# Optimization experiments

Measured on AMD Instinct MI355X. Metric: run time of the kernel, lower is better.

Reference implementation:

```python
import jax, jax.numpy as jnp
import numpy as np

N_NODES, E, M_CELLS = 100000, 400000, 50000
D_IN, D_H, D_OUT = 384, 256, 256


def setup_inputs() -> dict:
    key = jax.random.key(0)
    ks = jax.random.split(key, 13)
    s = 0.02
    return {
        "chunk_features": jax.random.normal(ks[0], (N_NODES, D_IN), jnp.float32),
        "flat_nodes_t": jax.random.randint(ks[1], (E,), 0, N_NODES),
        "cell_asgn_t": jax.random.randint(ks[2], (E,), 0, M_CELLS),
        "M": M_CELLS,
        # phi: Linear(D_IN,D_H)+ReLU, Linear(D_H,D_H)+ReLU
        "W1": jax.random.normal(ks[3], (D_IN, D_H), jnp.float32) * s,
        "b1": jnp.zeros((D_H,), jnp.float32),
        "W2": jax.random.normal(ks[4], (D_H, D_H), jnp.float32) * s,
        "b2": jnp.zeros((D_H,), jnp.float32),
        # rho: Linear(D_H,D_H)+ReLU, Linear(D_H,D_H)+ReLU, Linear(D_H,D_OUT)
        "R1": jax.random.normal(ks[5], (D_H, D_H), jnp.float32) * s,
        "c1": jnp.zeros((D_H,), jnp.float32),
        "R2": jax.random.normal(ks[6], (D_H, D_H), jnp.float32) * s,
        "c2": jnp.zeros((D_H,), jnp.float32),
        "R3": jax.random.normal(ks[7], (D_H, D_OUT), jnp.float32) * s,
        "c3": jnp.zeros((D_OUT,), jnp.float32),
    }


def reference(chunk_features, flat_nodes_t, cell_asgn_t, M,
              W1, b1, W2, b2, R1, c1, R2, c2, R3, c3):
    # gather node features per cell-membership: [E, D_IN]
    x = chunk_features[flat_nodes_t]
    # phi MLP
    h = jax.nn.relu(x @ W1 + b1)
    h = jax.nn.relu(h @ W2 + b2)            # [E, D_H]
    # scatter-add per cell (torch scatter_add_ into zeros)
    cell_sums = jax.ops.segment_sum(h, cell_asgn_t, num_segments=M)  # [M, D_H]
    # rho MLP
    r = jax.nn.relu(cell_sums @ R1 + c1)
    r = jax.nn.relu(r @ R2 + c2)
    return r @ R3 + c3                      # [M, D_OUT]
```

## Files before the change

kernel.cpp:

```cpp
#include <hip/hip_runtime.h>

typedef unsigned short u16;
typedef __bf16 bf16x8 __attribute__((ext_vector_type(8)));
typedef float f32x4 __attribute__((ext_vector_type(4)));

__device__ __forceinline__ u16 f2bf(float f) {
  unsigned int u = __builtin_bit_cast(unsigned int, f);
  u += 0x7fffu + ((u >> 16) & 1u);
  return (u16)(u >> 16);
}
__device__ __forceinline__ float bf2f(u16 h) {
  unsigned int u = ((unsigned int)h) << 16;
  return __builtin_bit_cast(float, u);
}

__global__ __launch_bounds__(256) void k_prep(
    const float* __restrict__ W1, const float* __restrict__ W2,
    const float* __restrict__ R1, const float* __restrict__ R2, const float* __restrict__ R3,
    u16* __restrict__ W1s, u16* __restrict__ W2s,
    u16* __restrict__ R1s, u16* __restrict__ R2s, u16* __restrict__ R3s) {
  int t = blockIdx.x * 256 + threadIdx.x;
  const float* src; u16* dst; int lt;
  if (t < 12288) { src = W1; dst = W1s; lt = t; }
  else {
    int u = t - 12288;
    int m = u >> 13;
    lt = u & 8191;
    if (m == 0)      { src = W2; dst = W2s; }
    else if (m == 1) { src = R1; dst = R1s; }
    else if (m == 2) { src = R2; dst = R2s; }
    else if (m == 3) { src = R3; dst = R3s; }
    else return;
  }
  int lane = lt & 63;
  int nt = (lt >> 6) & 15;
  int ks = lt >> 10;
  int col = nt * 16 + (lane & 15);
  int kb = ks * 32 + (lane >> 4) * 8;
  union { u16 u[8]; uint4 v; } o;
#pragma unroll
  for (int j = 0; j < 8; ++j) o.u[j] = f2bf(src[(size_t)(kb + j) * 256 + col]);
  *(uint4*)(dst + (size_t)lt * 8) = o.v;
}

__global__ __launch_bounds__(256) void k_hist(const int* __restrict__ cells,
                                              int* __restrict__ counts, int E) {
  int e = blockIdx.x * 256 + threadIdx.x;
  if (e < E) atomicAdd(&counts[cells[e]], 1);
}

__global__ __launch_bounds__(256) void k_scan1(const int* __restrict__ counts,
                                               int* __restrict__ offs,
                                               int* __restrict__ bsum, int M) {
  __shared__ int ws[4];
  int tid = threadIdx.x, lane = tid & 63, wid = tid >> 6;
  int i = blockIdx.x * 256 + tid;
  int v = (i < M) ? counts[i] : 0;
  int x = v;
#pragma unroll
  for (int s = 1; s < 64; s <<= 1) { int y = __shfl_up(x, s); if (lane >= s) x += y; }
  if (lane == 63) ws[wid] = x;
  __syncthreads();
  int pre = 0;
#pragma unroll
  for (int w = 0; w < 4; ++w) if (w < wid) pre += ws[w];
  if (i < M) offs[i] = pre + x - v;
  if (tid == 255) bsum[blockIdx.x] = pre + x;
}

__global__ __launch_bounds__(256) void k_scan2(int* __restrict__ bsum, int nb) {
  __shared__ int ws[4];
  int tid = threadIdx.x, lane = tid & 63, wid = tid >> 6;
  int v = (tid < nb) ? bsum[tid] : 0;
  int x = v;
#pragma unroll
  for (int s = 1; s < 64; s <<= 1) { int y = __shfl_up(x, s); if (lane >= s) x += y; }
  if (lane == 63) ws[wid] = x;
  __syncthreads();
  int pre = 0;
#pragma unroll
  for (int w = 0; w < 4; ++w) if (w < wid) pre += ws[w];
  if (tid < nb) bsum[tid] = pre + x - v;
}

__global__ __launch_bounds__(256) void k_scan3(int* __restrict__ offs,
                                               const int* __restrict__ bsum,
                                               int* __restrict__ cursor, int M, int E) {
  int i = blockIdx.x * 256 + threadIdx.x;
  if (i < M) { int o = offs[i] + bsum[blockIdx.x]; offs[i] = o; cursor[i] = o; }
  if (i == M) offs[M] = E;
}

__global__ __launch_bounds__(256) void k_scatter(const int* __restrict__ cells,
                                                 const int* __restrict__ nodes,
                                                 int* __restrict__ cursor,
                                                 int* __restrict__ sorted, int E) {
  int e = blockIdx.x * 256 + threadIdx.x;
  if (e < E) {
    int c = cells[e];
    int p = atomicAdd(&cursor[c], 1);
    sorted[p] = nodes[e];
  }
}

__global__ __launch_bounds__(256, 2) void k_phi(
    const float* __restrict__ X,
    const u16* __restrict__ W1s, const float* __restrict__ b1,
    const u16* __restrict__ W2s, const float* __restrict__ b2,
    u16* __restrict__ H, int N) {
  __shared__ __align__(16) u16 stage[64 * 256];
  __shared__ __align__(16) u16 hbuf[64 * 256];
  const int tid = threadIdx.x, lane = tid & 63, wid = tid >> 6;
  const int g = lane >> 4, r16 = lane & 15;
  const int rbase = blockIdx.x * 64;

  f32x4 acc[4][4];
#pragma unroll
  for (int m = 0; m < 4; ++m)
#pragma unroll
    for (int n = 0; n < 4; ++n) acc[m][n] = (f32x4){0.f, 0.f, 0.f, 0.f};

#pragma unroll
  for (int ph = 0; ph < 2; ++ph) {
    if (ph) __syncthreads();
    if (ph == 0) {
#pragma unroll
      for (int it = 0; it < 16; ++it) {
        int u = it * 256 + tid;
        int row = u >> 6, c4 = u & 63;
        int crow = rbase + row; crow = crow < N ? crow : N - 1;
        f32x4 v = *(const f32x4*)(X + (size_t)crow * 384 + c4 * 4);
        uint2 pk;
        pk.x = (unsigned int)f2bf(v[0]) | ((unsigned int)f2bf(v[1]) << 16);
        pk.y = (unsigned int)f2bf(v[2]) | ((unsigned int)f2bf(v[3]) << 16);
        *(uint2*)(stage + row * 256 + ((c4 * 4) ^ ((row & 15) << 3))) = pk;
      }
    } else {
#pragma unroll
      for (int it = 0; it < 8; ++it) {
        int u = it * 256 + tid;
        int row = u >> 5, c4 = u & 31;
        int crow = rbase + row; crow = crow < N ? crow : N - 1;
        f32x4 v = *(const f32x4*)(X + (size_t)crow * 384 + 256 + c4 * 4);
        uint2 pk;
        pk.x = (unsigned int)f2bf(v[0]) | ((unsigned int)f2bf(v[1]) << 16);
        pk.y = (unsigned int)f2bf(v[2]) | ((unsigned int)f2bf(v[3]) << 16);
        *(uint2*)(stage + row * 256 + ((c4 * 4) ^ ((row & 15) << 3))) = pk;
      }
    }
    __syncthreads();
    const int nks = ph ? 4 : 8;
    const int ksg0 = ph ? 8 : 0;
#pragma unroll
    for (int ksl = 0; ksl < nks; ++ksl) {
      int ks = ksg0 + ksl;
      bf16x8 bfr[4];
#pragma unroll
      for (int n = 0; n < 4; ++n)
        bfr[n] = *(const bf16x8*)(W1s + ((size_t)(ks * 16 + wid * 4 + n) * 64 + lane) * 8);
#pragma unroll
      for (int m = 0; m < 4; ++m) {
        int row = m * 16 + r16;
        bf16x8 af = *(const bf16x8*)(stage + row * 256 + ((ksl * 32 + g * 8) ^ (r16 << 3)));
#pragma unroll
        for (int n = 0; n < 4; ++n)
          acc[m][n] = __builtin_amdgcn_mfma_f32_16x16x32_bf16(af, bfr[n], acc[m][n], 0, 0, 0);
      }
    }
  }

  float bias1[4];
#pragma unroll
  for (int n = 0; n < 4; ++n) bias1[n] = b1[wid * 64 + n * 16 + r16];
#pragma unroll
  for (int m = 0; m < 4; ++m)
#pragma unroll
    for (int n = 0; n < 4; ++n)
#pragma unroll
      for (int rr = 0; rr < 4; ++rr) {
        int row = m * 16 + g * 4 + rr;
        int col = wid * 64 + n * 16 + r16;
        float v = fmaxf(acc[m][n][rr] + bias1[n], 0.f);
        hbuf[row * 256 + (col ^ ((row & 15) << 3))] = f2bf(v);
      }
  __syncthreads();

  f32x4 acc2[4][4];
#pragma unroll
  for (int m = 0; m < 4; ++m)
#pragma unroll
    for (int n = 0; n < 4; ++n) acc2[m][n] = (f32x4){0.f, 0.f, 0.f, 0.f};
#pragma unroll
  for (int ks = 0; ks < 8; ++ks) {
    bf16x8 bfr[4];
#pragma unroll
    for (int n = 0; n < 4; ++n)
      bfr[n] = *(const bf16x8*)(W2s + ((size_t)(ks * 16 + wid * 4 + n) * 64 + lane) * 8);
#pragma unroll
    for (int m = 0; m < 4; ++m) {
      int row = m * 16 + r16;
      bf16x8 af = *(const bf16x8*)(hbuf + row * 256 + ((ks * 32 + g * 8) ^ (r16 << 3)));
#pragma unroll
      for (int n = 0; n < 4; ++n)
        acc2[m][n] = __builtin_amdgcn_mfma_f32_16x16x32_bf16(af, bfr[n], acc2[m][n], 0, 0, 0);
    }
  }

  float bias2[4];
#pragma unroll
  for (int n = 0; n < 4; ++n) bias2[n] = b2[wid * 64 + n * 16 + r16];
#pragma unroll
  for (int m = 0; m < 4; ++m)
#pragma unroll
    for (int n = 0; n < 4; ++n)
#pragma unroll
      for (int rr = 0; rr < 4; ++rr) {
        int row = m * 16 + g * 4 + rr;
        int col = wid * 64 + n * 16 + r16;
        float v = fmaxf(acc2[m][n][rr] + bias2[n], 0.f);
        stage[row * 256 + (col ^ ((row & 15) << 3))] = f2bf(v);
      }
  __syncthreads();

#pragma unroll
  for (int it = 0; it < 8; ++it) {
    int u = it * 256 + tid;
    int row = u >> 5, k8 = u & 31;
    uint4 d = *(const uint4*)(stage + row * 256 + ((k8 * 8) ^ ((row & 15) << 3)));
    int grow = rbase + row;
    if (grow < N) *(uint4*)(H + (size_t)grow * 256 + k8 * 8) = d;
  }
}

__global__ __launch_bounds__(256) void k_cellsum(
    const u16* __restrict__ H, const int* __restrict__ sorted,
    const int* __restrict__ offs, u16* __restrict__ CS, int M) {
  const int lane = threadIdx.x & 63, wid = threadIdx.x >> 6;
  int c = blockIdx.x * 4 + wid;
  if (c >= M) return;
  int s = offs[c], e = offs[c + 1];
  float a0 = 0.f, a1 = 0.f, a2 = 0.f, a3 = 0.f;
  for (int i = s; i < e; ++i) {
    int node = sorted[i];
    ushort4 h = *(const ushort4*)(H + (size_t)node * 256 + lane * 4);
    a0 += bf2f(h.x); a1 += bf2f(h.y); a2 += bf2f(h.z); a3 += bf2f(h.w);
  }
  ushort4 o;
  o.x = f2bf(a0); o.y = f2bf(a1); o.z = f2bf(a2); o.w = f2bf(a3);
  *(ushort4*)(CS + (size_t)c * 256 + lane * 4) = o;
}

__global__ __launch_bounds__(256, 2) void k_rho(
    const u16* __restrict__ CS,
    const u16* __restrict__ R1s, const float* __restrict__ c1,
    const u16* __restrict__ R2s, const float* __restrict__ c2,
    const u16* __restrict__ R3s, const float* __restrict__ c3,
    float* __restrict__ OUT, int M) {
  __shared__ __align__(16) u16 stage[64 * 256];
  __shared__ __align__(16) u16 hbuf[64 * 256];
  const int tid = threadIdx.x, lane = tid & 63, wid = tid >> 6;
  const int g = lane >> 4, r16 = lane & 15;
  const int rbase = blockIdx.x * 64;

#pragma unroll
  for (int it = 0; it < 8; ++it) {
    int u = it * 256 + tid;
    int row = u >> 5, k8 = u & 31;
    int crow = rbase + row; crow = crow < M ? crow : M - 1;
    uint4 d = *(const uint4*)(CS + (size_t)crow * 256 + k8 * 8);
    *(uint4*)(stage + row * 256 + ((k8 * 8) ^ ((row & 15) << 3))) = d;
  }
  __syncthreads();

  f32x4 acc[4][4];
#pragma unroll
  for (int m = 0; m < 4; ++m)
#pragma unroll
    for (int n = 0; n < 4; ++n) acc[m][n] = (f32x4){0.f, 0.f, 0.f, 0.f};
#pragma unroll
  for (int ks = 0; ks < 8; ++ks) {
    bf16x8 bfr[4];
#pragma unroll
    for (int n = 0; n < 4; ++n)
      bfr[n] = *(const bf16x8*)(R1s + ((size_t)(ks * 16 + wid * 4 + n) * 64 + lane) * 8);
#pragma unroll
    for (int m = 0; m < 4; ++m) {
      int row = m * 16 + r16;
      bf16x8 af = *(const bf16x8*)(stage + row * 256 + ((ks * 32 + g * 8) ^ (r16 << 3)));
#pragma unroll
      for (int n = 0; n < 4; ++n)
        acc[m][n] = __builtin_amdgcn_mfma_f32_16x16x32_bf16(af, bfr[n], acc[m][n], 0, 0, 0);
    }
  }
  float bias1[4];
#pragma unroll
  for (int n = 0; n < 4; ++n) bias1[n] = c1[wid * 64 + n * 16 + r16];
#pragma unroll
  for (int m = 0; m < 4; ++m)
#pragma unroll
    for (int n = 0; n < 4; ++n)
#pragma unroll
      for (int rr = 0; rr < 4; ++rr) {
        int row = m * 16 + g * 4 + rr;
        int col = wid * 64 + n * 16 + r16;
        float v = fmaxf(acc[m][n][rr] + bias1[n], 0.f);
        hbuf[row * 256 + (col ^ ((row & 15) << 3))] = f2bf(v);
      }
  __syncthreads();

  f32x4 acc2[4][4];
#pragma unroll
  for (int m = 0; m < 4; ++m)
#pragma unroll
    for (int n = 0; n < 4; ++n) acc2[m][n] = (f32x4){0.f, 0.f, 0.f, 0.f};
#pragma unroll
  for (int ks = 0; ks < 8; ++ks) {
    bf16x8 bfr[4];
#pragma unroll
    for (int n = 0; n < 4; ++n)
      bfr[n] = *(const bf16x8*)(R2s + ((size_t)(ks * 16 + wid * 4 + n) * 64 + lane) * 8);
#pragma unroll
    for (int m = 0; m < 4; ++m) {
      int row = m * 16 + r16;
      bf16x8 af = *(const bf16x8*)(hbuf + row * 256 + ((ks * 32 + g * 8) ^ (r16 << 3)));
#pragma unroll
      for (int n = 0; n < 4; ++n)
        acc2[m][n] = __builtin_amdgcn_mfma_f32_16x16x32_bf16(af, bfr[n], acc2[m][n], 0, 0, 0);
    }
  }
  float bias2[4];
#pragma unroll
  for (int n = 0; n < 4; ++n) bias2[n] = c2[wid * 64 + n * 16 + r16];
#pragma unroll
  for (int m = 0; m < 4; ++m)
#pragma unroll
    for (int n = 0; n < 4; ++n)
#pragma unroll
      for (int rr = 0; rr < 4; ++rr) {
        int row = m * 16 + g * 4 + rr;
        int col = wid * 64 + n * 16 + r16;
        float v = fmaxf(acc2[m][n][rr] + bias2[n], 0.f);
        stage[row * 256 + (col ^ ((row & 15) << 3))] = f2bf(v);
      }
  __syncthreads();

  f32x4 acc3[4][4];
#pragma unroll
  for (int m = 0; m < 4; ++m)
#pragma unroll
    for (int n = 0; n < 4; ++n) acc3[m][n] = (f32x4){0.f, 0.f, 0.f, 0.f};
#pragma unroll
  for (int ks = 0; ks < 8; ++ks) {
    bf16x8 bfr[4];
#pragma unroll
    for (int n = 0; n < 4; ++n)
      bfr[n] = *(const bf16x8*)(R3s + ((size_t)(ks * 16 + wid * 4 + n) * 64 + lane) * 8);
#pragma unroll
    for (int m = 0; m < 4; ++m) {
      int row = m * 16 + r16;
      bf16x8 af = *(const bf16x8*)(stage + row * 256 + ((ks * 32 + g * 8) ^ (r16 << 3)));
#pragma unroll
      for (int n = 0; n < 4; ++n)
        acc3[m][n] = __builtin_amdgcn_mfma_f32_16x16x32_bf16(af, bfr[n], acc3[m][n], 0, 0, 0);
    }
  }
#pragma unroll
  for (int n = 0; n < 4; ++n) {
    float bias = c3[wid * 64 + n * 16 + r16];
#pragma unroll
    for (int m = 0; m < 4; ++m)
#pragma unroll
      for (int rr = 0; rr < 4; ++rr) {
        int grow = rbase + m * 16 + g * 4 + rr;
        if (grow < M) OUT[(size_t)grow * 256 + wid * 64 + n * 16 + r16] = acc3[m][n][rr] + bias;
      }
  }
}

extern "C" void kernel_launch(void* const* d_in, const int* in_sizes, int n_in,
                              void* d_out, int out_size, void* d_ws, size_t ws_size,
                              hipStream_t stream) {
  const float* X    = (const float*)d_in[0];
  const int* nodes  = (const int*)d_in[1];
  const int* cells  = (const int*)d_in[2];
  const float* W1   = (const float*)d_in[4];
  const float* b1   = (const float*)d_in[5];
  const float* W2   = (const float*)d_in[6];
  const float* b2   = (const float*)d_in[7];
  const float* R1   = (const float*)d_in[8];
  const float* c1   = (const float*)d_in[9];
  const float* R2   = (const float*)d_in[10];
  const float* c2   = (const float*)d_in[11];
  const float* R3   = (const float*)d_in[12];
  const float* c3   = (const float*)d_in[13];
  float* OUT = (float*)d_out;

  const int N = in_sizes[0] / 384;
  const int E = in_sizes[1];
  const int M = out_size / 256;

  char* ws = (char*)d_ws;
  size_t off = 0;
  auto alloc = [&](size_t b) { size_t o = off; off += (b + 255) & ~(size_t)255; return o; };
  u16* W1s    = (u16*)(ws + alloc((size_t)12 * 16 * 64 * 8 * 2));
  u16* W2s    = (u16*)(ws + alloc((size_t)8 * 16 * 64 * 8 * 2));
  u16* R1s    = (u16*)(ws + alloc((size_t)8 * 16 * 64 * 8 * 2));
  u16* R2s    = (u16*)(ws + alloc((size_t)8 * 16 * 64 * 8 * 2));
  u16* R3s    = (u16*)(ws + alloc((size_t)8 * 16 * 64 * 8 * 2));
  u16* H      = (u16*)(ws + alloc((size_t)N * 256 * 2));
  u16* CS     = (u16*)(ws + alloc((size_t)M * 256 * 2));
  int* counts = (int*)(ws + alloc((size_t)M * 4));
  int* offs   = (int*)(ws + alloc((size_t)(M + 1) * 4));
  int* cursor = (int*)(ws + alloc((size_t)M * 4));
  int* sorted = (int*)(ws + alloc((size_t)E * 4));
  int* bsum   = (int*)(ws + alloc((size_t)256 * 4));

  const int NB = (M + 255) / 256;

  hipMemsetAsync(counts, 0, (size_t)M * 4, stream);
  k_prep<<<176, 256, 0, stream>>>(W1, W2, R1, R2, R3, W1s, W2s, R1s, R2s, R3s);
  k_hist<<<(E + 255) / 256, 256, 0, stream>>>(cells, counts, E);
  k_scan1<<<NB, 256, 0, stream>>>(counts, offs, bsum, M);
  k_scan2<<<1, 256, 0, stream>>>(bsum, NB);
  k_scan3<<<(M + 256) / 256, 256, 0, stream>>>(offs, bsum, cursor, M, E);
  k_scatter<<<(E + 255) / 256, 256, 0, stream>>>(cells, nodes, cursor, sorted, E);
  k_phi<<<(N + 63) / 64, 256, 0, stream>>>(X, W1s, b1, W2s, b2, H, N);
  k_cellsum<<<(M + 3) / 4, 256, 0, stream>>>(H, sorted, offs, CS, M);
  k_rho<<<(M + 63) / 64, 256, 0, stream>>>(CS, R1s, c1, R2s, c2, R3s, c3, OUT, M);
}
```

Before: 232.6 us.

## Single LDS buffer, weight-fragment prefetch, and batched index gather in cellsum

```diff
diff --git a/kernel.cpp b/kernel.cpp
--- a/kernel.cpp
+++ b/kernel.cpp
@@ -103,71 +103,98 @@
   }
 }
 
-__global__ __launch_bounds__(256, 2) void k_phi(
+__global__ __launch_bounds__(256, 4) void k_phi(
     const float* __restrict__ X,
     const u16* __restrict__ W1s, const float* __restrict__ b1,
     const u16* __restrict__ W2s, const float* __restrict__ b2,
     u16* __restrict__ H, int N) {
-  __shared__ __align__(16) u16 stage[64 * 256];
-  __shared__ __align__(16) u16 hbuf[64 * 256];
+  __shared__ __align__(16) u16 buf[64 * 256];
   const int tid = threadIdx.x, lane = tid & 63, wid = tid >> 6;
   const int g = lane >> 4, r16 = lane & 15;
   const int rbase = blockIdx.x * 64;
 
+  const u16* w1p = W1s + (size_t)(wid * 4) * 512 + lane * 8;
+  const u16* w2p = W2s + (size_t)(wid * 4) * 512 + lane * 8;
+
   f32x4 acc[4][4];
 #pragma unroll
   for (int m = 0; m < 4; ++m)
 #pragma unroll
     for (int n = 0; n < 4; ++n) acc[m][n] = (f32x4){0.f, 0.f, 0.f, 0.f};
 
-#pragma unroll
-  for (int ph = 0; ph < 2; ++ph) {
-    if (ph) __syncthreads();
-    if (ph == 0) {
-#pragma unroll
-      for (int it = 0; it < 16; ++it) {
-        int u = it * 256 + tid;
-        int row = u >> 6, c4 = u & 63;
-        int crow = rbase + row; crow = crow < N ? crow : N - 1;
-        f32x4 v = *(const f32x4*)(X + (size_t)crow * 384 + c4 * 4);
-        uint2 pk;
-        pk.x = (unsigned int)f2bf(v[0]) | ((unsigned int)f2bf(v[1]) << 16);
-        pk.y = (unsigned int)f2bf(v[2]) | ((unsigned int)f2bf(v[3]) << 16);
-        *(uint2*)(stage + row * 256 + ((c4 * 4) ^ ((row & 15) << 3))) = pk;
-      }
+  bf16x8 bfr[4];
+#pragma unroll
+  for (int n = 0; n < 4; ++n) bfr[n] = *(const bf16x8*)(w1p + n * 512);
+
+#pragma unroll
+  for (int it = 0; it < 16; ++it) {
+    int u = it * 256 + tid;
+    int row = u >> 6, c4 = u & 63;
+    int crow = rbase + row; crow = crow < N ? crow : N - 1;
+    f32x4 v = *(const f32x4*)(X + (size_t)crow * 384 + c4 * 4);
+    uint2 pk;
+    pk.x = (unsigned int)f2bf(v[0]) | ((unsigned int)f2bf(v[1]) << 16);
+    pk.y = (unsigned int)f2bf(v[2]) | ((unsigned int)f2bf(v[3]) << 16);
+    *(uint2*)(buf + row * 256 + ((c4 * 4) ^ ((row & 15) << 3))) = pk;
+  }
+  __syncthreads();
+
+#pragma unroll
+  for (int ksl = 0; ksl < 8; ++ksl) {
+    bf16x8 bnx[4];
+#pragma unroll
+    for (int n = 0; n < 4; ++n)
+      bnx[n] = *(const bf16x8*)(w1p + (size_t)(ksl + 1) * 8192 + n * 512);
+#pragma unroll
+    for (int m = 0; m < 4; ++m) {
+      int row = m * 16 + r16;
+      bf16x8 af = *(const bf16x8*)(buf + row * 256 + ((ksl * 32 + g * 8) ^ (r16 << 3)));
+#pragma unroll
+      for (int n = 0; n < 4; ++n)
+        acc[m][n] = __builtin_amdgcn_mfma_f32_16x16x32_bf16(af, bfr[n], acc[m][n], 0, 0, 0);
+    }
+#pragma unroll
+    for (int n = 0; n < 4; ++n) bfr[n] = bnx[n];
+  }
+  __syncthreads();
+
+#pragma unroll
+  for (int it = 0; it < 8; ++it) {
+    int u = it * 256 + tid;
+    int row = u >> 5, c4 = u & 31;
+    int crow = rbase + row; crow = crow < N ? crow : N - 1;
+    f32x4 v = *(const f32x4*)(X + (size_t)crow * 384 + 256 + c4 * 4);
+    uint2 pk;
+    pk.x = (unsigned int)f2bf(v[0]) | ((unsigned int)f2bf(v[1]) << 16);
+    pk.y = (unsigned int)f2bf(v[2]) | ((unsigned int)f2bf(v[3]) << 16);
+    *(uint2*)(buf + row * 256 + ((c4 * 4) ^ ((row & 15) << 3))) = pk;
+  }
+  __syncthreads();
+
+#pragma unroll
+  for (int ksl = 0; ksl < 4; ++ksl) {
+    bf16x8 bnx[4];
+    if (ksl < 3) {
+#pragma unroll
+      for (int n = 0; n < 4; ++n)
+        bnx[n] = *(const bf16x8*)(w1p + (size_t)(9 + ksl) * 8192 + n * 512);
     } else {
 #pragma unroll
-      for (int it = 0; it < 8; ++it) {
-        int u = it * 256 + tid;
-        int row = u >> 5, c4 = u & 31;
-        int crow = rbase + row; crow = crow < N ? crow : N - 1;
-        f32x4 v = *(const f32x4*)(X + (size_t)crow * 384 + 256 + c4 * 4);
-        uint2 pk;
-        pk.x = (unsigned int)f2bf(v[0]) | ((unsigned int)f2bf(v[1]) << 16);
-        pk.y = (unsigned int)f2bf(v[2]) | ((unsigned int)f2bf(v[3]) << 16);
-        *(uint2*)(stage + row * 256 + ((c4 * 4) ^ ((row & 15) << 3))) = pk;
-      }
-    }
-    __syncthreads();
-    const int nks = ph ? 4 : 8;
-    const int ksg0 = ph ? 8 : 0;
-#pragma unroll
-    for (int ksl = 0; ksl < nks; ++ksl) {
-      int ks = ksg0 + ksl;
-      bf16x8 bfr[4];
-#pragma unroll
-      for (int n = 0; n < 4; ++n)
-        bfr[n] = *(const bf16x8*)(W1s + ((size_t)(ks * 16 + wid * 4 + n) * 64 + lane) * 8);
-#pragma unroll
-      for (int m = 0; m < 4; ++m) {
-        int row = m * 16 + r16;
-        bf16x8 af = *(const bf16x8*)(stage + row * 256 + ((ksl * 32 + g * 8) ^ (r16 << 3)));
-#pragma unroll
-        for (int n = 0; n < 4; ++n)
-          acc[m][n] = __builtin_amdgcn_mfma_f32_16x16x32_bf16(af, bfr[n], acc[m][n], 0, 0, 0);
-      }
-    }
-  }
+      for (int n = 0; n < 4; ++n)
+        bnx[n] = *(const bf16x8*)(w2p + n * 512);
+    }
+#pragma unroll
+    for (int m = 0; m < 4; ++m) {
+      int row = m * 16 + r16;
+      bf16x8 af = *(const bf16x8*)(buf + row * 256 + ((ksl * 32 + g * 8) ^ (r16 << 3)));
+#pragma unroll
+      for (int n = 0; n < 4; ++n)
+        acc[m][n] = __builtin_amdgcn_mfma_f32_16x16x32_bf16(af, bfr[n], acc[m][n], 0, 0, 0);
+    }
+#pragma unroll
+    for (int n = 0; n < 4; ++n) bfr[n] = bnx[n];
+  }
+  __syncthreads();
 
   float bias1[4];
 #pragma unroll
@@ -181,7 +208,7 @@
         int row = m * 16 + g * 4 + rr;
         int col = wid * 64 + n * 16 + r16;
         float v = fmaxf(acc[m][n][rr] + bias1[n], 0.f);
-        hbuf[row * 256 + (col ^ ((row & 15) << 3))] = f2bf(v);
+        buf[row * 256 + (col ^ ((row & 15) << 3))] = f2bf(v);
       }
   __syncthreads();
 
@@ -192,19 +219,26 @@
     for (int n = 0; n < 4; ++n) acc2[m][n] = (f32x4){0.f, 0.f, 0.f, 0.f};
 #pragma unroll
   for (int ks = 0; ks < 8; ++ks) {
-    bf16x8 bfr[4];
-#pragma unroll
-    for (int n = 0; n < 4; ++n)
-      bfr[n] = *(const bf16x8*)(W2s + ((size_t)(ks * 16 + wid * 4 + n) * 64 + lane) * 8);
+    bf16x8 bnx[4];
+    if (ks < 7) {
+#pragma unroll
+      for (int n = 0; n < 4; ++n)
+        bnx[n] = *(const bf16x8*)(w2p + (size_t)(ks + 1) * 8192 + n * 512);
+    }
 #pragma unroll
     for (int m = 0; m < 4; ++m) {
       int row = m * 16 + r16;
-      bf16x8 af = *(const bf16x8*)(hbuf + row * 256 + ((ks * 32 + g * 8) ^ (r16 << 3)));
+      bf16x8 af = *(const bf16x8*)(buf + row * 256 + ((ks * 32 + g * 8) ^ (r16 << 3)));
 #pragma unroll
       for (int n = 0; n < 4; ++n)
         acc2[m][n] = __builtin_amdgcn_mfma_f32_16x16x32_bf16(af, bfr[n], acc2[m][n], 0, 0, 0);
     }
-  }
+    if (ks < 7) {
+#pragma unroll
+      for (int n = 0; n < 4; ++n) bfr[n] = bnx[n];
+    }
+  }
+  __syncthreads();
 
   float bias2[4];
 #pragma unroll
@@ -218,7 +252,7 @@
         int row = m * 16 + g * 4 + rr;
         int col = wid * 64 + n * 16 + r16;
         float v = fmaxf(acc2[m][n][rr] + bias2[n], 0.f);
-        stage[row * 256 + (col ^ ((row & 15) << 3))] = f2bf(v);
+        buf[row * 256 + (col ^ ((row & 15) << 3))] = f2bf(v);
       }
   __syncthreads();
 
@@ -226,7 +260,7 @@
   for (int it = 0; it < 8; ++it) {
     int u = it * 256 + tid;
     int row = u >> 5, k8 = u & 31;
-    uint4 d = *(const uint4*)(stage + row * 256 + ((k8 * 8) ^ ((row & 15) << 3)));
+    uint4 d = *(const uint4*)(buf + row * 256 + ((k8 * 8) ^ ((row & 15) << 3)));
     int grow = rbase + row;
     if (grow < N) *(uint4*)(H + (size_t)grow * 256 + k8 * 8) = d;
   }
@@ -240,27 +274,51 @@
   if (c >= M) return;
   int s = offs[c], e = offs[c + 1];
   float a0 = 0.f, a1 = 0.f, a2 = 0.f, a3 = 0.f;
-  for (int i = s; i < e; ++i) {
-    int node = sorted[i];
-    ushort4 h = *(const ushort4*)(H + (size_t)node * 256 + lane * 4);
-    a0 += bf2f(h.x); a1 += bf2f(h.y); a2 += bf2f(h.z); a3 += bf2f(h.w);
+  for (int base = s; base < e; base += 64) {
+    int cnt = e - base; if (cnt > 64) cnt = 64;
+    int idx = sorted[base + (lane < cnt ? lane : 0)];
+    int j = 0;
+    for (; j + 4 <= cnt; j += 4) {
+      int n0 = __shfl(idx, j), n1 = __shfl(idx, j + 1);
+      int n2 = __shfl(idx, j + 2), n3 = __shfl(idx, j + 3);
+      ushort4 h0 = *(const ushort4*)(H + (size_t)n0 * 256 + lane * 4);
+      ushort4 h1 = *(const ushort4*)(H + (size_t)n1 * 256 + lane * 4);
+      ushort4 h2 = *(const ushort4*)(H + (size_t)n2 * 256 + lane * 4);
+      ushort4 h3 = *(const ushort4*)(H + (size_t)n3 * 256 + lane * 4);
+      a0 += bf2f(h0.x) + bf2f(h1.x) + bf2f(h2.x) + bf2f(h3.x);
+      a1 += bf2f(h0.y) + bf2f(h1.y) + bf2f(h2.y) + bf2f(h3.y);
+      a2 += bf2f(h0.z) + bf2f(h1.z) + bf2f(h2.z) + bf2f(h3.z);
+      a3 += bf2f(h0.w) + bf2f(h1.w) + bf2f(h2.w) + bf2f(h3.w);
+    }
+    for (; j < cnt; ++j) {
+      int nd = __shfl(idx, j);
+      ushort4 h = *(const ushort4*)(H + (size_t)nd * 256 + lane * 4);
+      a0 += bf2f(h.x); a1 += bf2f(h.y); a2 += bf2f(h.z); a3 += bf2f(h.w);
+    }
   }
   ushort4 o;
   o.x = f2bf(a0); o.y = f2bf(a1); o.z = f2bf(a2); o.w = f2bf(a3);
   *(ushort4*)(CS + (size_t)c * 256 + lane * 4) = o;
 }
 
-__global__ __launch_bounds__(256, 2) void k_rho(
+__global__ __launch_bounds__(256, 4) void k_rho(
     const u16* __restrict__ CS,
     const u16* __restrict__ R1s, const float* __restrict__ c1,
     const u16* __restrict__ R2s, const float* __restrict__ c2,
     const u16* __restrict__ R3s, const float* __restrict__ c3,
     float* __restrict__ OUT, int M) {
-  __shared__ __align__(16) u16 stage[64 * 256];
-  __shared__ __align__(16) u16 hbuf[64 * 256];
+  __shared__ __align__(16) u16 buf[64 * 256];
   const int tid = threadIdx.x, lane = tid & 63, wid = tid >> 6;
   const int g = lane >> 4, r16 = lane & 15;
   const int rbase = blockIdx.x * 64;
+
+  const u16* w1p = R1s + (size_t)(wid * 4) * 512 + lane * 8;
+  const u16* w2p = R2s + (size_t)(wid * 4) * 512 + lane * 8;
+  const u16* w3p = R3s + (size_t)(wid * 4) * 512 + lane * 8;
+
+  bf16x8 bfr[4];
+#pragma unroll
+  for (int n = 0; n < 4; ++n) bfr[n] = *(const bf16x8*)(w1p + n * 512);
 
 #pragma unroll
   for (int it = 0; it < 8; ++it) {
@@ -268,7 +326,7 @@
     int row = u >> 5, k8 = u & 31;
     int crow = rbase + row; crow = crow < M ? crow : M - 1;
     uint4 d = *(const uint4*)(CS + (size_t)crow * 256 + k8 * 8);
-    *(uint4*)(stage + row * 256 + ((k8 * 8) ^ ((row & 15) << 3))) = d;
+    *(uint4*)(buf + row * 256 + ((k8 * 8) ^ ((row & 15) << 3))) = d;
   }
   __syncthreads();
 
@@ -279,19 +337,29 @@
     for (int n = 0; n < 4; ++n) acc[m][n] = (f32x4){0.f, 0.f, 0.f, 0.f};
 #pragma unroll
   for (int ks = 0; ks < 8; ++ks) {
-    bf16x8 bfr[4];
-#pragma unroll
-    for (int n = 0; n < 4; ++n)
-      bfr[n] = *(const bf16x8*)(R1s + ((size_t)(ks * 16 + wid * 4 + n) * 64 + lane) * 8);
+    bf16x8 bnx[4];
+    if (ks < 7) {
+#pragma unroll
+      for (int n = 0; n < 4; ++n)
+        bnx[n] = *(const bf16x8*)(w1p + (size_t)(ks + 1) * 8192 + n * 512);
+    } else {
+#pragma unroll
+      for (int n = 0; n < 4; ++n)
+        bnx[n] = *(const bf16x8*)(w2p + n * 512);
+    }
 #pragma unroll
     for (int m = 0; m < 4; ++m) {
       int row = m * 16 + r16;
-      bf16x8 af = *(const bf16x8*)(stage + row * 256 + ((ks * 32 + g * 8) ^ (r16 << 3)));
+      bf16x8 af = *(const bf16x8*)(buf + row * 256 + ((ks * 32 + g * 8) ^ (r16 << 3)));
 #pragma unroll
       for (int n = 0; n < 4; ++n)
         acc[m][n] = __builtin_amdgcn_mfma_f32_16x16x32_bf16(af, bfr[n], acc[m][n], 0, 0, 0);
     }
-  }
+#pragma unroll
+    for (int n = 0; n < 4; ++n) bfr[n] = bnx[n];
+  }
+  __syncthreads();
+
   float bias1[4];
 #pragma unroll
   for (int n = 0; n < 4; ++n) bias1[n] = c1[wid * 64 + n * 16 + r16];
@@ -304,7 +372,7 @@
         int row = m * 16 + g * 4 + rr;
         int col = wid * 64 + n * 16 + r16;
         float v = fmaxf(acc[m][n][rr] + bias1[n], 0.f);
-        hbuf[row * 256 + (col ^ ((row & 15) << 3))] = f2bf(v);
+        buf[row * 256 + (col ^ ((row & 15) << 3))] = f2bf(v);
       }
   __syncthreads();
 
@@ -315,19 +383,29 @@
     for (int n = 0; n < 4; ++n) acc2[m][n] = (f32x4){0.f, 0.f, 0.f, 0.f};
 #pragma unroll
   for (int ks = 0; ks < 8; ++ks) {
-    bf16x8 bfr[4];
-#pragma unroll
-    for (int n = 0; n < 4; ++n)
-      bfr[n] = *(const bf16x8*)(R2s + ((size_t)(ks * 16 + wid * 4 + n) * 64 + lane) * 8);
+    bf16x8 bnx[4];
+    if (ks < 7) {
+#pragma unroll
+      for (int n = 0; n < 4; ++n)
+        bnx[n] = *(const bf16x8*)(w2p + (size_t)(ks + 1) * 8192 + n * 512);
+    } else {
+#pragma unroll
+      for (int n = 0; n < 4; ++n)
+        bnx[n] = *(const bf16x8*)(w3p + n * 512);
+    }
 #pragma unroll
     for (int m = 0; m < 4; ++m) {
       int row = m * 16 + r16;
-      bf16x8 af = *(const bf16x8*)(hbuf + row * 256 + ((ks * 32 + g * 8) ^ (r16 << 3)));
+      bf16x8 af = *(const bf16x8*)(buf + row * 256 + ((ks * 32 + g * 8) ^ (r16 << 3)));
 #pragma unroll
       for (int n = 0; n < 4; ++n)
         acc2[m][n] = __builtin_amdgcn_mfma_f32_16x16x32_bf16(af, bfr[n], acc2[m][n], 0, 0, 0);
     }
-  }
+#pragma unroll
+    for (int n = 0; n < 4; ++n) bfr[n] = bnx[n];
+  }
+  __syncthreads();
+
   float bias2[4];
 #pragma unroll
   for (int n = 0; n < 4; ++n) bias2[n] = c2[wid * 64 + n * 16 + r16];
@@ -340,7 +418,7 @@
         int row = m * 16 + g * 4 + rr;
         int col = wid * 64 + n * 16 + r16;
         float v = fmaxf(acc2[m][n][rr] + bias2[n], 0.f);
-        stage[row * 256 + (col ^ ((row & 15) << 3))] = f2bf(v);
+        buf[row * 256 + (col ^ ((row & 15) << 3))] = f2bf(v);
       }
   __syncthreads();
 
@@ -351,17 +429,23 @@
     for (int n = 0; n < 4; ++n) acc3[m][n] = (f32x4){0.f, 0.f, 0.f, 0.f};
 #pragma unroll
   for (int ks = 0; ks < 8; ++ks) {
-    bf16x8 bfr[4];
-#pragma unroll
-    for (int n = 0; n < 4; ++n)
-      bfr[n] = *(const bf16x8*)(R3s + ((size_t)(ks * 16 + wid * 4 + n) * 64 + lane) * 8);
+    bf16x8 bnx[4];
+    if (ks < 7) {
+#pragma unroll
+      for (int n = 0; n < 4; ++n)
+        bnx[n] = *(const bf16x8*)(w3p + (size_t)(ks + 1) * 8192 + n * 512);
+    }
 #pragma unroll
     for (int m = 0; m < 4; ++m) {
       int row = m * 16 + r16;
-      bf16x8 af = *(const bf16x8*)(stage + row * 256 + ((ks * 32 + g * 8) ^ (r16 << 3)));
+      bf16x8 af = *(const bf16x8*)(buf + row * 256 + ((ks * 32 + g * 8) ^ (r16 << 3)));
 #pragma unroll
       for (int n = 0; n < 4; ++n)
         acc3[m][n] = __builtin_amdgcn_mfma_f32_16x16x32_bf16(af, bfr[n], acc3[m][n], 0, 0, 0);
+    }
+    if (ks < 7) {
+#pragma unroll
+      for (int n = 0; n < 4; ++n) bfr[n] = bnx[n];
     }
   }
 #pragma unroll
```

After: 263.7 us. 1.13x slower.
